# Optimization experiments

Hardware: AMD Instinct MI355X
Metric: run time of the kernel (lower is better)

Reference implementation:

```python
import math
import jax, jax.numpy as jnp
import numpy as np

B, N = 1, 512
C_S, C_Z, H, C, P_Q, P_V = 384, 128, 12, 16, 4, 8
CAT = C_Z * H + C * H + 3 * H * P_V + 1  # 2017


def _apply(t_r, t_t, x):
    # t_r: (b,n,3,3), t_t: (b,n,3), x: (b,3,h,p,n) -> global frame coords
    xg = jnp.einsum('bnij,bjhpn->bihpn', t_r, x)
    return xg + jnp.swapaxes(t_t, 1, 2)[:, :, None, None, :]


def setup_inputs() -> dict:
    key = jax.random.key(0)
    ks = jax.random.split(key, 14)
    f = lambda k, shp: jax.random.normal(k, shp, dtype=jnp.float32)
    return {
        's': f(ks[0], (B, C_S, N)),
        'z': f(ks[1], (B, C_Z, N, N)),
        't_r': f(ks[2], (B, N, 3, 3)),
        't_t': f(ks[3], (B, N, 3)),
        'Wq': f(ks[4], (C * H, C_S)) * 0.02,
        'Wk': f(ks[5], (C * H, C_S)) * 0.02,
        'Wv': f(ks[6], (C * H, C_S)) * 0.02,
        'Wqp': f(ks[7], (3 * H * P_Q, C_S)) * 0.02,
        'Wkp': f(ks[8], (3 * H * P_Q, C_S)) * 0.02,
        'Wvp': f(ks[9], (3 * H * P_V, C_S)) * 0.02,
        'Wb': f(ks[10], (H, C_Z)) * 0.02,
        'gamma': f(ks[11], (H, 1, 1)) * 0.5,
        'Ws': f(ks[12], (C_S, CAT)) * 0.02,
        'bs': jnp.zeros((C_S,), dtype=jnp.float32),
    }


def reference(s, z, t_r, t_t, Wq, Wk, Wv, Wqp, Wkp, Wvp, Wb, gamma, Ws, bs):
    b, _, n = s.shape
    w_c = math.sqrt(2.0 / (9.0 * P_Q))
    w_l = math.sqrt(1.0 / 3.0)

    proj = lambda W: jnp.einsum('oc,bcn->bon', W, s)
    # torch rearrange 'b (c h) i -> b c h i' == reshape(b, c, h, n)
    q = proj(Wq).reshape(b, C, H, n)
    k = proj(Wk).reshape(b, C, H, n)
    v = proj(Wv).reshape(b, C, H, n)
    qp = proj(Wqp).reshape(b, 3, H, P_Q, n)
    kp = proj(Wkp).reshape(b, 3, H, P_Q, n)
    vp = proj(Wvp).reshape(b, 3, H, P_V, n)

    qg = _apply(t_r, t_t, qp)  # (b,3,h,p,n)
    kg = _apply(t_r, t_t, kp)
    diff = qg[..., :, None] - kg[..., None, :]          # (b,3,h,p,n,n)
    dist2 = jnp.sum(diff * diff, axis=(1, 3))           # sum coords + points -> (b,h,n,n)
    tmp = jax.nn.softplus(gamma)[None] * (w_c / 2.0) * dist2

    b_bias = jnp.einsum('hc,bcij->bhij', Wb, z)
    qk = jnp.einsum('bchi,bchj->bhij', q, k) / math.sqrt(C)
    a = jax.nn.softmax(w_l * (qk + b_bias - tmp), axis=-1)  # (b,h,n,n)

    o1 = jnp.einsum('bhij,bcij->bchi', a, z).reshape(b, C_Z * H, n)
    o2 = jnp.einsum('bhij,bchj->bchi', a, v).reshape(b, C * H, n)

    vg = _apply(t_r, t_t, vp)                           # (b,3,h,pv,n)
    o3g = jnp.einsum('bhij,bchpj->bchpi', a, vg)        # (b,3,h,pv,n)
    t_r_inv = jnp.swapaxes(t_r, -1, -2)
    t_t_inv = jnp.einsum('bnij,bnj->bni', -t_r_inv, t_t)
    o3 = _apply(t_r_inv, t_t_inv, o3g).reshape(b, 3 * H * P_V, n)
    o3_norm = jnp.linalg.norm(o3, axis=1, keepdims=True)  # (b,1,n)

    cat = jnp.concatenate([o1, o2, o3, o3_norm], axis=1)  # (b, CAT, n)
    return jnp.einsum('oc,bcn->bon', Ws, cat) + bs[None, :, None]
```

## Files before the change

kernel.cpp:

```cpp
#include <hip/hip_runtime.h>
#include <math.h>

#define N 512
#define H 12
#define CC 16
#define CZ 128
#define CS 384
#define PQ 4
#define PV 8
#define CATR 2017

__global__ __launch_bounds__(256) void k_proj(
    const float* __restrict__ s,
    const float* __restrict__ Wq, const float* __restrict__ Wk, const float* __restrict__ Wv,
    const float* __restrict__ Wqp, const float* __restrict__ Wkp, const float* __restrict__ Wvp,
    float* __restrict__ proj)
{
    __shared__ float Wt[16][33];
    __shared__ float St[32][128];
    int t = threadIdx.x;
    int o0 = blockIdx.x * 16;
    int n0 = blockIdx.y * 128;
    const float* Wsrc; int orow;
    if (o0 < 192)      { Wsrc = Wq;  orow = o0; }
    else if (o0 < 384) { Wsrc = Wk;  orow = o0-192; }
    else if (o0 < 576) { Wsrc = Wv;  orow = o0-384; }
    else if (o0 < 720) { Wsrc = Wqp; orow = o0-576; }
    else if (o0 < 864) { Wsrc = Wkp; orow = o0-720; }
    else               { Wsrc = Wvp; orow = o0-864; }

    int og = t >> 6, nl = t & 63;
    float acc[4][2] = {};
    for (int c0 = 0; c0 < CS; c0 += 32) {
        __syncthreads();
        for (int k = 0; k < 2; k++) {
            int idx = t + k*256;
            int oo = idx >> 5, ccol = idx & 31;
            Wt[oo][ccol] = Wsrc[(orow+oo)*CS + c0 + ccol];
        }
        for (int k = 0; k < 4; k++) {
            int idx = t + k*256;
            int ccr = idx >> 5, nn4 = idx & 31;
            float4 v = *(const float4*)&s[(c0+ccr)*N + n0 + nn4*4];
            *(float4*)&St[ccr][nn4*4] = v;
        }
        __syncthreads();
        for (int kk = 0; kk < 32; kk++) {
            float sv0 = St[kk][nl], sv1 = St[kk][nl+64];
            #pragma unroll
            for (int r = 0; r < 4; r++) {
                float w = Wt[og*4+r][kk];
                acc[r][0] += w * sv0;
                acc[r][1] += w * sv1;
            }
        }
    }
    for (int r = 0; r < 4; r++) {
        int o = o0 + og*4 + r;
        proj[o*N + n0 + nl]      = acc[r][0];
        proj[o*N + n0 + 64 + nl] = acc[r][1];
    }
}

__global__ void k_frames(const float* __restrict__ proj,
                         const float* __restrict__ t_r, const float* __restrict__ t_t,
                         float* __restrict__ qg, float* __restrict__ kg, float* __restrict__ vg)
{
    int gid = blockIdx.x * blockDim.x + threadIdx.x;
    int n = gid & (N-1);
    int hp = gid >> 9;
    if (hp >= 192) return;
    const float* src; float* dst; int rowb, stride;
    if (hp < 48)      { src = proj + 576*N; dst = qg; rowb = hp;    stride = 48; }
    else if (hp < 96) { src = proj + 720*N; dst = kg; rowb = hp-48; stride = 48; }
    else              { src = proj + 864*N; dst = vg; rowb = hp-96; stride = 96; }
    float x0 = src[(rowb + 0*stride)*N + n];
    float x1 = src[(rowb + 1*stride)*N + n];
    float x2 = src[(rowb + 2*stride)*N + n];
    #pragma unroll
    for (int d = 0; d < 3; d++) {
        float r0 = t_r[(n*3+d)*3+0], r1 = t_r[(n*3+d)*3+1], r2 = t_r[(n*3+d)*3+2];
        dst[(rowb + d*stride)*N + n] = r0*x0 + r1*x1 + r2*x2 + t_t[n*3+d];
    }
}

__global__ void k_sq(const float* __restrict__ qg, const float* __restrict__ kg,
                     float* __restrict__ sq_q, float* __restrict__ sq_k)
{
    int gid = blockIdx.x * blockDim.x + threadIdx.x;
    int n = gid & (N-1);
    int sel = gid >> 9;
    int h = sel % H;
    const float* g = (sel < H) ? qg : kg;
    float* outp = (sel < H) ? sq_q : sq_k;
    float acc = 0.f;
    #pragma unroll
    for (int d = 0; d < 3; d++)
        #pragma unroll
        for (int p = 0; p < PQ; p++) {
            float v = g[(size_t)((d*H + h)*PQ + p)*N + n];
            acc += v*v;
        }
    outp[h*N + n] = acc;
}

__global__ __launch_bounds__(256) void k_attn(
    const float* __restrict__ z, const float* __restrict__ proj,
    const float* __restrict__ qg, const float* __restrict__ kg,
    const float* __restrict__ sq_q, const float* __restrict__ sq_k,
    const float* __restrict__ Wb, const float* __restrict__ gamma,
    float* __restrict__ a)
{
    int i = blockIdx.x;
    int t = threadIdx.x;
    int j0 = t*2;
    const float w_l  = 0.57735026918962584f;
    const float w_c2 = 0.11785113019775793f;

    float ch[H];
    #pragma unroll
    for (int h = 0; h < H; h++) {
        float g = gamma[h];
        float sp = (g > 20.f) ? g : log1pf(expf(g));
        ch[h] = sp * w_c2;
    }

    float acc[H][2] = {};
    const float* q = proj;
    const float* k = proj + 192*N;

    for (int c = 0; c < CZ; c++) {
        float2 zz = *(const float2*)&z[((size_t)c*N + i)*N + j0];
        #pragma unroll
        for (int h = 0; h < H; h++) {
            float w = Wb[h*CZ + c];
            acc[h][0] += w*zz.x; acc[h][1] += w*zz.y;
        }
    }
    for (int c = 0; c < CC; c++) {
        #pragma unroll
        for (int h = 0; h < H; h++) {
            float qv = 0.25f * q[(size_t)(c*H+h)*N + i];
            float2 kk = *(const float2*)&k[(size_t)(c*H+h)*N + j0];
            acc[h][0] += qv*kk.x; acc[h][1] += qv*kk.y;
        }
    }
    for (int dp = 0; dp < 3*PQ; dp++) {
        int d = dp >> 2, p = dp & 3;
        #pragma unroll
        for (int h = 0; h < H; h++) {
            int row = (d*H+h)*PQ + p;
            float qv = 2.f*ch[h]*qg[(size_t)row*N + i];
            float2 kk = *(const float2*)&kg[(size_t)row*N + j0];
            acc[h][0] += qv*kk.x; acc[h][1] += qv*kk.y;
        }
    }
    float logit[H][2];
    #pragma unroll
    for (int h = 0; h < H; h++) {
        float sqq = sq_q[h*N + i];
        float2 sk = *(const float2*)&sq_k[h*N + j0];
        logit[h][0] = w_l*(acc[h][0] - ch[h]*(sqq + sk.x));
        logit[h][1] = w_l*(acc[h][1] - ch[h]*(sqq + sk.y));
    }

    __shared__ float red[2][H][4];
    int wv = t >> 6, lane = t & 63;
    #pragma unroll
    for (int h = 0; h < H; h++) {
        float m = fmaxf(logit[h][0], logit[h][1]);
        for (int sft = 32; sft > 0; sft >>= 1) m = fmaxf(m, __shfl_xor(m, sft));
        if (lane == 0) red[0][h][wv] = m;
    }
    __syncthreads();
    #pragma unroll
    for (int h = 0; h < H; h++) {
        float m = fmaxf(fmaxf(red[0][h][0], red[0][h][1]), fmaxf(red[0][h][2], red[0][h][3]));
        float e0 = __expf(logit[h][0]-m), e1 = __expf(logit[h][1]-m);
        logit[h][0] = e0; logit[h][1] = e1;
        float sm = e0 + e1;
        for (int sft = 32; sft > 0; sft >>= 1) sm += __shfl_xor(sm, sft);
        if (lane == 0) red[1][h][wv] = sm;
    }
    __syncthreads();
    #pragma unroll
    for (int h = 0; h < H; h++) {
        float sm = red[1][h][0]+red[1][h][1]+red[1][h][2]+red[1][h][3];
        float inv = 1.f/sm;
        float2 o; o.x = logit[h][0]*inv; o.y = logit[h][1]*inv;
        *(float2*)&a[((size_t)h*N + i)*N + j0] = o;
    }
}

__global__ __launch_bounds__(256) void k_o1(
    const float* __restrict__ z, const float* __restrict__ a, float* __restrict__ cat)
{
    __shared__ float als[H*516];
    __shared__ float zls[128*66];
    int i = blockIdx.x;
    int t = threadIdx.x;
    int c0 = (t >> 2)*2;
    int h0 = (t & 3)*3;
    for (int k = 0; k < 6; k++) {
        int idx = t + k*256;
        int h = idx >> 7, j4 = idx & 127;
        float4 v = *(const float4*)&a[((size_t)h*N + i)*N + j4*4];
        *(float4*)&als[h*516 + j4*4] = v;
    }
    float acc[2][3] = {};
    for (int jc = 0; jc < 8; jc++) {
        __syncthreads();
        for (int k = 0; k < 16; k++) {
            int idx = t + k*256;
            int c = idx >> 5, j2 = idx & 31;
            float2 v = *(const float2*)&z[((size_t)c*N + i)*N + jc*64 + j2*2];
            *(float2*)&zls[c*66 + j2*2] = v;
        }
        __syncthreads();
        for (int jj = 0; jj < 64; jj++) {
            float z0 = zls[c0*66 + jj], z1 = zls[(c0+1)*66 + jj];
            float a0 = als[h0*516 + jc*64 + jj];
            float a1 = als[(h0+1)*516 + jc*64 + jj];
            float a2 = als[(h0+2)*516 + jc*64 + jj];
            acc[0][0] += z0*a0; acc[0][1] += z0*a1; acc[0][2] += z0*a2;
            acc[1][0] += z1*a0; acc[1][1] += z1*a1; acc[1][2] += z1*a2;
        }
    }
    #pragma unroll
    for (int cc = 0; cc < 2; cc++)
        #pragma unroll
        for (int hh = 0; hh < 3; hh++)
            cat[(size_t)((c0+cc)*H + h0+hh)*N + i] = acc[cc][hh];
}

__global__ __launch_bounds__(256) void k_o2o3g(
    const float* __restrict__ a, const float* __restrict__ proj, const float* __restrict__ vg,
    float* __restrict__ cat, float* __restrict__ o3g)
{
    __shared__ float ats[32*66];
    __shared__ float vts[40*66];
    int h = blockIdx.x, i0 = blockIdx.y*32;
    int t = threadIdx.x;
    int il = t & 31, rg = t >> 5;
    const float* v = proj + 384*N;
    float acc[5] = {};
    for (int jc = 0; jc < 8; jc++) {
        __syncthreads();
        for (int k = 0; k < 4; k++) {
            int idx = t + k*256;
            int ii = idx >> 5, j2 = idx & 31;
            *(float2*)&ats[ii*66 + j2*2] =
                *(const float2*)&a[((size_t)h*N + i0+ii)*N + jc*64 + j2*2];
        }
        for (int idx = t; idx < 1280; idx += 256) {
            int r = idx >> 5, j2 = idx & 31;
            const float* src;
            if (r < 16) src = v + (size_t)(r*H + h)*N;
            else { int rr = r-16; int e = rr >> 3, p = rr & 7;
                   src = vg + (size_t)((e*H+h)*PV + p)*N; }
            *(float2*)&vts[r*66 + j2*2] = *(const float2*)&src[jc*64 + j2*2];
        }
        __syncthreads();
        for (int jj = 0; jj < 64; jj++) {
            float av = ats[il*66 + jj];
            #pragma unroll
            for (int r = 0; r < 5; r++)
                acc[r] += av * vts[(rg*5+r)*66 + jj];
        }
    }
    #pragma unroll
    for (int r = 0; r < 5; r++) {
        int row = rg*5 + r;
        if (row < 16) cat[(size_t)(1536 + row*H + h)*N + i0 + il] = acc[r];
        else { int rr = row-16; int e = rr >> 3, p = rr & 7;
               o3g[(size_t)((e*H+h)*PV + p)*N + i0 + il] = acc[r]; }
    }
}

__global__ void k_o3(const float* __restrict__ o3g,
                     const float* __restrict__ t_r, const float* __restrict__ t_t,
                     float* __restrict__ cat)
{
    int gid = blockIdx.x*blockDim.x + threadIdx.x;
    int i = gid & (N-1), hp = gid >> 9;
    if (hp >= 96) return;
    float x0 = o3g[(size_t)(0*96 + hp)*N + i] - t_t[i*3+0];
    float x1 = o3g[(size_t)(1*96 + hp)*N + i] - t_t[i*3+1];
    float x2 = o3g[(size_t)(2*96 + hp)*N + i] - t_t[i*3+2];
    #pragma unroll
    for (int d = 0; d < 3; d++) {
        float o = t_r[(i*3+0)*3+d]*x0 + t_r[(i*3+1)*3+d]*x1 + t_r[(i*3+2)*3+d]*x2;
        cat[(size_t)(1728 + d*96 + hp)*N + i] = o;
    }
}

__global__ void k_norm(float* __restrict__ cat)
{
    int i = blockIdx.x*blockDim.x + threadIdx.x;
    if (i >= N) return;
    float acc = 0.f;
    for (int r = 0; r < 288; r++) {
        float v = cat[(size_t)(1728+r)*N + i];
        acc += v*v;
    }
    cat[(size_t)2016*N + i] = sqrtf(acc);
}

__global__ __launch_bounds__(256) void k_final(
    const float* __restrict__ Ws, const float* __restrict__ bs,
    const float* __restrict__ cat, float* __restrict__ out)
{
    __shared__ float Wt[16*33];
    __shared__ float Ct[32*66];
    int o0 = blockIdx.x*16, n0 = blockIdx.y*64;
    int ks = blockIdx.z;
    int kbeg = ks*505, kend = min(CATR, kbeg+505);
    int t = threadIdx.x;
    int og = t >> 6, nl = t & 63;
    float acc[4] = {};
    for (int c0 = kbeg; c0 < kend; c0 += 32) {
        __syncthreads();
        for (int k = 0; k < 2; k++) {
            int idx = t + k*256;
            int oo = idx >> 5, ccol = idx & 31;
            int c = c0 + ccol;
            Wt[oo*33 + ccol] = (c < kend) ? Ws[(size_t)(o0+oo)*CATR + c] : 0.f;
        }
        for (int k = 0; k < 4; k++) {
            int idx = t + k*256;
            int ccr = idx >> 5, j2 = idx & 31;
            int c = c0 + ccr;
            float2 vv; vv.x = 0.f; vv.y = 0.f;
            if (c < kend) vv = *(const float2*)&cat[(size_t)c*N + n0 + j2*2];
            *(float2*)&Ct[ccr*66 + j2*2] = vv;
        }
        __syncthreads();
        int klim = min(32, kend - c0);
        for (int kk = 0; kk < klim; kk++) {
            float cv = Ct[kk*66 + nl];
            #pragma unroll
            for (int r = 0; r < 4; r++)
                acc[r] += Wt[(og*4+r)*33 + kk] * cv;
        }
    }
    #pragma unroll
    for (int r = 0; r < 4; r++) {
        int o = o0 + og*4 + r;
        float val = acc[r];
        if (ks == 0) val += bs[o];
        atomicAdd(&out[(size_t)o*N + n0 + nl], val);
    }
}

extern "C" void kernel_launch(void* const* d_in, const int* in_sizes, int n_in,
                              void* d_out, int out_size, void* d_ws, size_t ws_size,
                              hipStream_t stream)
{
    const float* s     = (const float*)d_in[0];
    const float* z     = (const float*)d_in[1];
    const float* t_r   = (const float*)d_in[2];
    const float* t_t   = (const float*)d_in[3];
    const float* Wq    = (const float*)d_in[4];
    const float* Wk    = (const float*)d_in[5];
    const float* Wv    = (const float*)d_in[6];
    const float* Wqp   = (const float*)d_in[7];
    const float* Wkp   = (const float*)d_in[8];
    const float* Wvp   = (const float*)d_in[9];
    const float* Wb    = (const float*)d_in[10];
    const float* gamma = (const float*)d_in[11];
    const float* Ws    = (const float*)d_in[12];
    const float* bs    = (const float*)d_in[13];
    float* out = (float*)d_out;

    float* ws   = (float*)d_ws;
    float* proj = ws;
    float* qg   = proj + 1152*N;
    float* kg   = qg   + 144*N;
    float* vg   = kg   + 144*N;
    float* sq_q = vg   + 288*N;
    float* sq_k = sq_q + H*N;
    float* o3g  = sq_k + H*N;
    float* a    = o3g  + 288*N;
    float* cat  = a    + (size_t)H*N*N;

    k_proj  <<<dim3(72,4),  256, 0, stream>>>(s, Wq, Wk, Wv, Wqp, Wkp, Wvp, proj);
    k_frames<<<384,         256, 0, stream>>>(proj, t_r, t_t, qg, kg, vg);
    k_sq    <<<48,          256, 0, stream>>>(qg, kg, sq_q, sq_k);
    k_attn  <<<512,         256, 0, stream>>>(z, proj, qg, kg, sq_q, sq_k, Wb, gamma, a);
    k_o1    <<<512,         256, 0, stream>>>(z, a, cat);
    k_o2o3g <<<dim3(12,16), 256, 0, stream>>>(a, proj, vg, cat, o3g);
    k_o3    <<<192,         256, 0, stream>>>(o3g, t_r, t_t, cat);
    k_norm  <<<2,           256, 0, stream>>>(cat);
    hipMemsetAsync(out, 0, (size_t)CS*N*sizeof(float), stream);
    k_final <<<dim3(24,8,4),256, 0, stream>>>(Ws, bs, cat, out);
}
```

Before: 445.7 us.

## Split reduction across thread halves with float4 loads in attention kernels

Three kernels are restructured. In k_attn each thread now covers four columns, and the two halves of the block each reduce half of the channel dimension, then combine through shared memory. k_o1 and k_o2o3g move to float4 shared-memory tiles with the j-reduction split across two halves followed by a shared-memory combine, and k_o2o3g now launches twice as many blocks with smaller i tiles. The aim is more memory-level parallelism and wider loads, at the cost of more shared memory, extra syncs, and half the threads sitting idle during the softmax.

```diff
diff --git a/kernel.cpp b/kernel.cpp
--- a/kernel.cpp
+++ b/kernel.cpp
@@ -111,9 +111,13 @@
     const float* __restrict__ Wb, const float* __restrict__ gamma,
     float* __restrict__ a)
 {
+    __shared__ float redbuf[128*52];
+    __shared__ float sred[2][H][2];
     int i = blockIdx.x;
     int t = threadIdx.x;
-    int j0 = t*2;
+    int half = t >> 7;
+    int jl = t & 127;
+    int j4 = jl * 4;
     const float w_l  = 0.57735026918962584f;
     const float w_c2 = 0.11785113019775793f;
 
@@ -125,70 +129,109 @@
         ch[h] = sp * w_c2;
     }
 
-    float acc[H][2] = {};
-    const float* q = proj;
-    const float* k = proj + 192*N;
-
-    for (int c = 0; c < CZ; c++) {
-        float2 zz = *(const float2*)&z[((size_t)c*N + i)*N + j0];
+    float acc[H][4] = {};
+
+    {
+        const float* zi = z + (size_t)i * N;
+        int cbeg = half * 64;
+        for (int c = cbeg; c < cbeg + 64; c += 4) {
+            float4 z0 = *(const float4*)&zi[(size_t)(c+0)*N*N + j4];
+            float4 z1 = *(const float4*)&zi[(size_t)(c+1)*N*N + j4];
+            float4 z2 = *(const float4*)&zi[(size_t)(c+2)*N*N + j4];
+            float4 z3 = *(const float4*)&zi[(size_t)(c+3)*N*N + j4];
+            #pragma unroll
+            for (int h = 0; h < H; h++) {
+                float w0 = Wb[h*CZ + c+0], w1 = Wb[h*CZ + c+1];
+                float w2 = Wb[h*CZ + c+2], w3 = Wb[h*CZ + c+3];
+                acc[h][0] += w0*z0.x + w1*z1.x + w2*z2.x + w3*z3.x;
+                acc[h][1] += w0*z0.y + w1*z1.y + w2*z2.y + w3*z3.y;
+                acc[h][2] += w0*z0.z + w1*z1.z + w2*z2.z + w3*z3.z;
+                acc[h][3] += w0*z0.w + w1*z1.w + w2*z2.w + w3*z3.w;
+            }
+        }
+    }
+
+    {
+        const float* q = proj;
+        const float* k = proj + 192*N;
+        for (int c = half*8; c < half*8 + 8; c++) {
+            #pragma unroll
+            for (int h = 0; h < H; h++) {
+                int r = c*H + h;
+                float qv = 0.25f * q[(size_t)r*N + i];
+                float4 k4 = *(const float4*)&k[(size_t)r*N + j4];
+                acc[h][0] += qv*k4.x; acc[h][1] += qv*k4.y;
+                acc[h][2] += qv*k4.z; acc[h][3] += qv*k4.w;
+            }
+        }
+    }
+
+    {
+        for (int dp = half; dp < 12; dp += 2) {
+            int d = dp >> 2, p = dp & 3;
+            #pragma unroll
+            for (int h = 0; h < H; h++) {
+                int r = (d*H + h)*PQ + p;
+                float qv = 2.f * ch[h] * qg[(size_t)r*N + i];
+                float4 k4 = *(const float4*)&kg[(size_t)r*N + j4];
+                acc[h][0] += qv*k4.x; acc[h][1] += qv*k4.y;
+                acc[h][2] += qv*k4.z; acc[h][3] += qv*k4.w;
+            }
+        }
+    }
+
+    if (half == 1) {
+        #pragma unroll
+        for (int h = 0; h < H; h++)
+            *(float4*)&redbuf[jl*52 + h*4] = *(float4*)&acc[h][0];
+    }
+    __syncthreads();
+    if (half == 0) {
         #pragma unroll
         for (int h = 0; h < H; h++) {
-            float w = Wb[h*CZ + c];
-            acc[h][0] += w*zz.x; acc[h][1] += w*zz.y;
-        }
-    }
-    for (int c = 0; c < CC; c++) {
+            float4 o = *(const float4*)&redbuf[jl*52 + h*4];
+            acc[h][0] += o.x; acc[h][1] += o.y; acc[h][2] += o.z; acc[h][3] += o.w;
+        }
         #pragma unroll
         for (int h = 0; h < H; h++) {
-            float qv = 0.25f * q[(size_t)(c*H+h)*N + i];
-            float2 kk = *(const float2*)&k[(size_t)(c*H+h)*N + j0];
-            acc[h][0] += qv*kk.x; acc[h][1] += qv*kk.y;
-        }
-    }
-    for (int dp = 0; dp < 3*PQ; dp++) {
-        int d = dp >> 2, p = dp & 3;
+            float s0 = sq_q[h*N + i];
+            float4 sk = *(const float4*)&sq_k[h*N + j4];
+            acc[h][0] = w_l*(acc[h][0] - ch[h]*(s0 + sk.x));
+            acc[h][1] = w_l*(acc[h][1] - ch[h]*(s0 + sk.y));
+            acc[h][2] = w_l*(acc[h][2] - ch[h]*(s0 + sk.z));
+            acc[h][3] = w_l*(acc[h][3] - ch[h]*(s0 + sk.w));
+        }
+        int wv = t >> 6, lane = t & 63;
         #pragma unroll
         for (int h = 0; h < H; h++) {
-            int row = (d*H+h)*PQ + p;
-            float qv = 2.f*ch[h]*qg[(size_t)row*N + i];
-            float2 kk = *(const float2*)&kg[(size_t)row*N + j0];
-            acc[h][0] += qv*kk.x; acc[h][1] += qv*kk.y;
-        }
-    }
-    float logit[H][2];
-    #pragma unroll
-    for (int h = 0; h < H; h++) {
-        float sqq = sq_q[h*N + i];
-        float2 sk = *(const float2*)&sq_k[h*N + j0];
-        logit[h][0] = w_l*(acc[h][0] - ch[h]*(sqq + sk.x));
-        logit[h][1] = w_l*(acc[h][1] - ch[h]*(sqq + sk.y));
-    }
-
-    __shared__ float red[2][H][4];
-    int wv = t >> 6, lane = t & 63;
-    #pragma unroll
-    for (int h = 0; h < H; h++) {
-        float m = fmaxf(logit[h][0], logit[h][1]);
-        for (int sft = 32; sft > 0; sft >>= 1) m = fmaxf(m, __shfl_xor(m, sft));
-        if (lane == 0) red[0][h][wv] = m;
-    }
-    __syncthreads();
-    #pragma unroll
-    for (int h = 0; h < H; h++) {
-        float m = fmaxf(fmaxf(red[0][h][0], red[0][h][1]), fmaxf(red[0][h][2], red[0][h][3]));
-        float e0 = __expf(logit[h][0]-m), e1 = __expf(logit[h][1]-m);
-        logit[h][0] = e0; logit[h][1] = e1;
-        float sm = e0 + e1;
-        for (int sft = 32; sft > 0; sft >>= 1) sm += __shfl_xor(sm, sft);
-        if (lane == 0) red[1][h][wv] = sm;
-    }
-    __syncthreads();
-    #pragma unroll
-    for (int h = 0; h < H; h++) {
-        float sm = red[1][h][0]+red[1][h][1]+red[1][h][2]+red[1][h][3];
-        float inv = 1.f/sm;
-        float2 o; o.x = logit[h][0]*inv; o.y = logit[h][1]*inv;
-        *(float2*)&a[((size_t)h*N + i)*N + j0] = o;
+            float m = fmaxf(fmaxf(acc[h][0], acc[h][1]), fmaxf(acc[h][2], acc[h][3]));
+            for (int s = 32; s > 0; s >>= 1) m = fmaxf(m, __shfl_xor(m, s));
+            if (lane == 0) sred[0][h][wv] = m;
+        }
+    }
+    __syncthreads();
+    if (half == 0) {
+        int wv = t >> 6, lane = t & 63;
+        #pragma unroll
+        for (int h = 0; h < H; h++) {
+            float m = fmaxf(sred[0][h][0], sred[0][h][1]);
+            acc[h][0] = __expf(acc[h][0]-m); acc[h][1] = __expf(acc[h][1]-m);
+            acc[h][2] = __expf(acc[h][2]-m); acc[h][3] = __expf(acc[h][3]-m);
+            float sm = acc[h][0]+acc[h][1]+acc[h][2]+acc[h][3];
+            for (int s = 32; s > 0; s >>= 1) sm += __shfl_xor(sm, s);
+            if (lane == 0) sred[1][h][wv] = sm;
+        }
+    }
+    __syncthreads();
+    if (half == 0) {
+        #pragma unroll
+        for (int h = 0; h < H; h++) {
+            float inv = 1.f / (sred[1][h][0] + sred[1][h][1]);
+            float4 o;
+            o.x = acc[h][0]*inv; o.y = acc[h][1]*inv;
+            o.z = acc[h][2]*inv; o.w = acc[h][3]*inv;
+            *(float4*)&a[((size_t)h*N + i)*N + j4] = o;
+        }
     }
 }
 
@@ -196,84 +239,123 @@
     const float* __restrict__ z, const float* __restrict__ a, float* __restrict__ cat)
 {
     __shared__ float als[H*516];
-    __shared__ float zls[128*66];
+    __shared__ float zls[128*68];
     int i = blockIdx.x;
     int t = threadIdx.x;
-    int c0 = (t >> 2)*2;
-    int h0 = (t & 3)*3;
+    int cg = t & 31, hg = (t>>5)&3, jh = t>>7;
+
     for (int k = 0; k < 6; k++) {
         int idx = t + k*256;
-        int h = idx >> 7, j4 = idx & 127;
-        float4 v = *(const float4*)&a[((size_t)h*N + i)*N + j4*4];
-        *(float4*)&als[h*516 + j4*4] = v;
-    }
-    float acc[2][3] = {};
+        int h = idx >> 7, jj4 = idx & 127;
+        *(float4*)&als[h*516 + jj4*4] = *(const float4*)&a[((size_t)h*N + i)*N + jj4*4];
+    }
+    float acc[4][3] = {};
     for (int jc = 0; jc < 8; jc++) {
         __syncthreads();
-        for (int k = 0; k < 16; k++) {
-            int idx = t + k*256;
-            int c = idx >> 5, j2 = idx & 31;
-            float2 v = *(const float2*)&z[((size_t)c*N + i)*N + jc*64 + j2*2];
-            *(float2*)&zls[c*66 + j2*2] = v;
-        }
-        __syncthreads();
-        for (int jj = 0; jj < 64; jj++) {
-            float z0 = zls[c0*66 + jj], z1 = zls[(c0+1)*66 + jj];
-            float a0 = als[h0*516 + jc*64 + jj];
-            float a1 = als[(h0+1)*516 + jc*64 + jj];
-            float a2 = als[(h0+2)*516 + jc*64 + jj];
-            acc[0][0] += z0*a0; acc[0][1] += z0*a1; acc[0][2] += z0*a2;
-            acc[1][0] += z1*a0; acc[1][1] += z1*a1; acc[1][2] += z1*a2;
-        }
-    }
-    #pragma unroll
-    for (int cc = 0; cc < 2; cc++)
-        #pragma unroll
-        for (int hh = 0; hh < 3; hh++)
-            cat[(size_t)((c0+cc)*H + h0+hh)*N + i] = acc[cc][hh];
+        for (int k = 0; k < 8; k++) {
+            int idx = t + k*256;
+            int c = idx >> 4, j4 = idx & 15;
+            *(float4*)&zls[c*68 + j4*4] =
+                *(const float4*)&z[((size_t)c*N + i)*N + jc*64 + j4*4];
+        }
+        __syncthreads();
+        int jb = jh * 32;
+        #pragma unroll
+        for (int s = 0; s < 8; s++) {
+            int jo = jb + s*4;
+            float4 a0 = *(const float4*)&als[(hg*3+0)*516 + jc*64 + jo];
+            float4 a1 = *(const float4*)&als[(hg*3+1)*516 + jc*64 + jo];
+            float4 a2 = *(const float4*)&als[(hg*3+2)*516 + jc*64 + jo];
+            #pragma unroll
+            for (int r = 0; r < 4; r++) {
+                float4 zz = *(const float4*)&zls[(cg + 32*r)*68 + jo];
+                acc[r][0] += zz.x*a0.x + zz.y*a0.y + zz.z*a0.z + zz.w*a0.w;
+                acc[r][1] += zz.x*a1.x + zz.y*a1.y + zz.z*a1.z + zz.w*a1.w;
+                acc[r][2] += zz.x*a2.x + zz.y*a2.y + zz.z*a2.z + zz.w*a2.w;
+            }
+        }
+    }
+    __syncthreads();
+    if (jh == 1) {
+        float* rb = zls + (t & 127)*13;
+        #pragma unroll
+        for (int r = 0; r < 4; r++)
+            #pragma unroll
+            for (int hh = 0; hh < 3; hh++) rb[r*3+hh] = acc[r][hh];
+    }
+    __syncthreads();
+    if (jh == 0) {
+        const float* rb = zls + t*13;
+        #pragma unroll
+        for (int r = 0; r < 4; r++)
+            #pragma unroll
+            for (int hh = 0; hh < 3; hh++) acc[r][hh] += rb[r*3+hh];
+        #pragma unroll
+        for (int r = 0; r < 4; r++)
+            #pragma unroll
+            for (int hh = 0; hh < 3; hh++) {
+                int c = cg + 32*r, h = hg*3 + hh;
+                cat[(size_t)(c*H + h)*N + i] = acc[r][hh];
+            }
+    }
 }
 
 __global__ __launch_bounds__(256) void k_o2o3g(
     const float* __restrict__ a, const float* __restrict__ proj, const float* __restrict__ vg,
     float* __restrict__ cat, float* __restrict__ o3g)
 {
-    __shared__ float ats[32*66];
-    __shared__ float vts[40*66];
-    int h = blockIdx.x, i0 = blockIdx.y*32;
+    __shared__ float ats[16*132];
+    __shared__ float vts[40*132];
+    int h = blockIdx.x, i0 = blockIdx.y*16;
     int t = threadIdx.x;
-    int il = t & 31, rg = t >> 5;
+    int il = t & 15, rg = (t>>4)&7, jh = t>>7;
     const float* v = proj + 384*N;
     float acc[5] = {};
-    for (int jc = 0; jc < 8; jc++) {
-        __syncthreads();
-        for (int k = 0; k < 4; k++) {
-            int idx = t + k*256;
-            int ii = idx >> 5, j2 = idx & 31;
-            *(float2*)&ats[ii*66 + j2*2] =
-                *(const float2*)&a[((size_t)h*N + i0+ii)*N + jc*64 + j2*2];
+    for (int jc = 0; jc < 4; jc++) {
+        __syncthreads();
+        for (int k = 0; k < 2; k++) {
+            int idx = t + k*256;
+            int ii = idx >> 5, j4 = idx & 31;
+            *(float4*)&ats[ii*132 + j4*4] =
+                *(const float4*)&a[((size_t)h*N + i0+ii)*N + jc*128 + j4*4];
         }
         for (int idx = t; idx < 1280; idx += 256) {
-            int r = idx >> 5, j2 = idx & 31;
-            const float* src;
-            if (r < 16) src = v + (size_t)(r*H + h)*N;
-            else { int rr = r-16; int e = rr >> 3, p = rr & 7;
-                   src = vg + (size_t)((e*H+h)*PV + p)*N; }
-            *(float2*)&vts[r*66 + j2*2] = *(const float2*)&src[jc*64 + j2*2];
-        }
-        __syncthreads();
-        for (int jj = 0; jj < 64; jj++) {
-            float av = ats[il*66 + jj];
-            #pragma unroll
-            for (int r = 0; r < 5; r++)
-                acc[r] += av * vts[(rg*5+r)*66 + jj];
-        }
-    }
-    #pragma unroll
-    for (int r = 0; r < 5; r++) {
-        int row = rg*5 + r;
-        if (row < 16) cat[(size_t)(1536 + row*H + h)*N + i0 + il] = acc[r];
-        else { int rr = row-16; int e = rr >> 3, p = rr & 7;
-               o3g[(size_t)((e*H+h)*PV + p)*N + i0 + il] = acc[r]; }
+            int r = idx >> 5, j4 = idx & 31;
+            const float* src = (r < 16) ? (v + (size_t)(r*H + h)*N)
+                : (vg + (size_t)(((r-16)>>3)*96 + h*PV + ((r-16)&7))*N);
+            *(float4*)&vts[r*132 + j4*4] = *(const float4*)&src[jc*128 + j4*4];
+        }
+        __syncthreads();
+        int jb = jh * 64;
+        #pragma unroll
+        for (int s = 0; s < 16; s++) {
+            int jo = jb + s*4;
+            float4 a4 = *(const float4*)&ats[il*132 + jo];
+            #pragma unroll
+            for (int r = 0; r < 5; r++) {
+                float4 v4 = *(const float4*)&vts[(rg*5+r)*132 + jo];
+                acc[r] += v4.x*a4.x + v4.y*a4.y + v4.z*a4.z + v4.w*a4.w;
+            }
+        }
+    }
+    __syncthreads();
+    if (jh == 1) {
+        float* rb = ats + (t & 127)*6;
+        #pragma unroll
+        for (int r = 0; r < 5; r++) rb[r] = acc[r];
+    }
+    __syncthreads();
+    if (jh == 0) {
+        const float* rb = ats + t*6;
+        #pragma unroll
+        for (int r = 0; r < 5; r++) acc[r] += rb[r];
+        #pragma unroll
+        for (int r = 0; r < 5; r++) {
+            int row = rg*5 + r;
+            if (row < 16) cat[(size_t)(1536 + row*H + h)*N + i0 + il] = acc[r];
+            else { int rr = row - 16;
+                   o3g[(size_t)((rr>>3)*96 + h*PV + (rr&7))*N + i0 + il] = acc[r]; }
+        }
     }
 }
 
@@ -388,7 +470,7 @@
     k_sq    <<<48,          256, 0, stream>>>(qg, kg, sq_q, sq_k);
     k_attn  <<<512,         256, 0, stream>>>(z, proj, qg, kg, sq_q, sq_k, Wb, gamma, a);
     k_o1    <<<512,         256, 0, stream>>>(z, a, cat);
-    k_o2o3g <<<dim3(12,16), 256, 0, stream>>>(a, proj, vg, cat, o3g);
+    k_o2o3g <<<dim3(12,32), 256, 0, stream>>>(a, proj, vg, cat, o3g);
     k_o3    <<<192,         256, 0, stream>>>(o3g, t_r, t_t, cat);
     k_norm  <<<2,           256, 0, stream>>>(cat);
     hipMemsetAsync(out, 0, (size_t)CS*N*sizeof(float), stream);
```

Measured after the change: 416.4 us. -6.6%, faster.
